# Performance work log

Hardware: AMD Instinct MI355X
Metric: run time of the kernel (lower is better)

Reference implementation:

```python
import jax, jax.numpy as jnp
import numpy as np

NEG = -9e15

def setup_inputs() -> dict:
    key = jax.random.key(0)
    k1, k2, k3, k4 = jax.random.split(key, 4)
    N, F_IN, F_OUT = 8192, 256, 256
    h = jax.random.normal(k1, (N, F_IN), dtype=jnp.float32)
    adj = jax.random.randint(k2, (N, N), 0, 2, dtype=jnp.int32)
    W = jax.random.normal(k3, (F_IN, F_OUT), dtype=jnp.float32) * (1.0 / np.sqrt(F_IN))
    a = jax.random.normal(k4, (2 * F_OUT,), dtype=jnp.float32) * (1.0 / np.sqrt(2 * F_OUT))
    return {"h": h, "adj": adj, "W": W, "a": a}

def reference(h, adj, W, a):
    # Wh: [N, F_out]
    Wh = h @ W
    F_OUT = Wh.shape[1]
    a1, a2 = a[:F_OUT], a[F_OUT:]
    # cat-based score decomposes: e_ij = leaky_relu(a1.Wh_i + a2.Wh_j)
    s1 = Wh @ a1  # [N]
    s2 = Wh @ a2  # [N]
    e = jax.nn.leaky_relu(s1[:, None] + s2[None, :], negative_slope=0.2)  # [N, N]
    e = jnp.where(adj > 0, e, NEG)
    attention = jax.nn.softmax(e, axis=-1)
    # dropout is identity in eval mode
    return attention @ Wh
```

## Files before the change

kernel.cpp:

```cpp
#include <hip/hip_runtime.h>

typedef short s8v  __attribute__((ext_vector_type(8)));
typedef float f4v  __attribute__((ext_vector_type(4)));
typedef int   v4i  __attribute__((ext_vector_type(4)));
typedef float v4f  __attribute__((ext_vector_type(4)));
typedef int   v2i  __attribute__((ext_vector_type(2)));

#define NNODES 8192
#define FDIM   256
#define NJC    4
#define JLEN   2048
#define TROWS  32
#define KSTEP  32
#define NSTEP  64

__device__ __forceinline__ float bf2f(unsigned short u) {
    unsigned int x = ((unsigned int)u) << 16;
    return __builtin_bit_cast(float, x);
}
__device__ __forceinline__ unsigned short f2bf(float f) {
    unsigned int x = __builtin_bit_cast(unsigned int, f);
    x += 0x7fffu + ((x >> 16) & 1u);
    return (unsigned short)(x >> 16);
}
__device__ __forceinline__ int cvt_pk(float lo, float hi) {
    int r;
    asm("v_cvt_pk_bf16_f32 %0, %1, %2" : "=v"(r) : "v"(lo), "v"(hi));
    return r;
}

__device__ __forceinline__ void barrier_lds_only() {
    asm volatile("s_waitcnt lgkmcnt(0)" ::: "memory");
    __builtin_amdgcn_s_barrier();
    asm volatile("" ::: "memory");
}

__global__ __launch_bounds__(256) void prep_kernel(const float* __restrict__ W,
                                                   const float* __restrict__ a,
                                                   unsigned short* __restrict__ WT,
                                                   float* __restrict__ v1,
                                                   float* __restrict__ v2) {
    if (blockIdx.x < 256) {
        int idx = blockIdx.x * 256 + threadIdx.x;
        int r = idx >> 8, c = idx & 255;
        WT[c * 256 + r] = f2bf(W[r * 256 + c]);
    } else {
        __shared__ float r1[256], r2[256];
        int b = blockIdx.x - 256, n = threadIdx.x;
        float w = W[(size_t)b * FDIM + n];
        r1[n] = w * a[n];
        r2[n] = w * a[FDIM + n];
        __syncthreads();
        for (int off = 128; off > 0; off >>= 1) {
            if (n < off) { r1[n] += r1[n + off]; r2[n] += r2[n + off]; }
            __syncthreads();
        }
        if (n == 0) { v1[b] = r1[0]; v2[b] = r2[0]; }
    }
}

__global__ __launch_bounds__(128) void wh_kernel(
    const float* __restrict__ h, const unsigned short* __restrict__ WT,
    const float* __restrict__ v1, const float* __restrict__ v2,
    unsigned short* __restrict__ PB,
    float* __restrict__ s1, float* __restrict__ s2)
{
    __shared__ float v1_lds[FDIM], v2_lds[FDIM];
    int tid = threadIdx.x;
    v1_lds[tid] = v1[tid];       v1_lds[tid + 128] = v1[tid + 128];
    v2_lds[tid] = v2[tid];       v2_lds[tid + 128] = v2[tid + 128];
    __syncthreads();

    int w = tid >> 6, lane = tid & 63, q = lane >> 4, l15 = lane & 15;
    int i_base = blockIdx.x * 32 + w * 16;

    f4v acc[16] = {};
    float s1p = 0.f, s2p = 0.f;

    for (int k0 = 0; k0 < 256; k0 += 32) {
        const float* hp = h + (size_t)(i_base + l15) * FDIM + k0 + q * 8;
        f4v h0 = *(const f4v*)hp;
        f4v h1 = *(const f4v*)(hp + 4);
        union { v4i u; s8v s; } af;
        af.u[0] = cvt_pk(h0[0], h0[1]);
        af.u[1] = cvt_pk(h0[2], h0[3]);
        af.u[2] = cvt_pk(h1[0], h1[1]);
        af.u[3] = cvt_pk(h1[2], h1[3]);
#pragma unroll
        for (int j = 0; j < 4; ++j) {
            s1p += h0[j] * v1_lds[k0 + q * 8 + j] + h1[j] * v1_lds[k0 + q * 8 + 4 + j];
            s2p += h0[j] * v2_lds[k0 + q * 8 + j] + h1[j] * v2_lds[k0 + q * 8 + 4 + j];
        }
#pragma unroll
        for (int t = 0; t < 16; ++t) {
            s8v bf = *(const s8v*)(WT + (size_t)(t * 16 + l15) * FDIM + k0 + q * 8);
            acc[t] = __builtin_amdgcn_mfma_f32_16x16x32_bf16(af.s, bf, acc[t], 0, 0, 0);
        }
    }

    s1p += __shfl_xor(s1p, 16, 64);
    s1p += __shfl_xor(s1p, 32, 64);
    s2p += __shfl_xor(s2p, 16, 64);
    s2p += __shfl_xor(s2p, 32, 64);
    if (lane < 16) {
        s1[i_base + lane] = s1p;
        s2[i_base + lane] = s2p;
    }

#pragma unroll
    for (int t = 0; t < 16; ++t) {
        int i0 = i_base + q * 4;
        size_t a16 = (size_t)((i0 >> 5) * 16 + t) * 512
                   + l15 * 32 + ((i0 >> 3) & 3) * 8 + (i0 & 7);
        v2i pk;
        pk[0] = cvt_pk(acc[t][0], acc[t][1]);
        pk[1] = cvt_pk(acc[t][2], acc[t][3]);
        *(v2i*)(PB + a16) = pk;
    }
}

__global__ __launch_bounds__(256, 4) void attn_partial(
    const int* __restrict__ adj, const unsigned short* __restrict__ PB,
    const float* __restrict__ s1, const float* __restrict__ s2,
    float* __restrict__ Npart, float* __restrict__ dpart)
{
    __shared__ float s2_lds[JLEN];
    __shared__ unsigned short P_lds[2][TROWS * KSTEP];
    __shared__ float dsum_lds[TROWS][8];

    int tid = threadIdx.x;
    int jc = blockIdx.x & 3, rt = blockIdx.x >> 2;
    int j0 = jc * JLEN;

    for (int i = tid; i < JLEN / 4; i += 256)
        ((v4f*)s2_lds)[i] = ((const v4f*)(s2 + j0))[i];

    int m = tid >> 3, idx = tid & 7;
    int row_g = rt * TROWS + m;
    float s1v = s1[row_g];
    const int* arow = adj + (size_t)row_g * NNODES + j0 + idx * 4;
    int q_w = idx >> 1, half = idx & 1;
    int woff = (((q_w * 32 + m) * 8 + half * 4)) ^ (q_w * 16);

    int g = tid >> 6, lane = tid & 63, q = lane >> 4, l15 = lane & 15;
    const unsigned short* pbb = PB + (size_t)(jc * 64) * 16 * 512 + l15 * 32 + q * 8;

    f4v acc[2][4] = {};
    float dsum = 0.0f;

    __syncthreads();

    v4i p0 = __builtin_nontemporal_load((const v4i*)(arow));
    v4i a1 = __builtin_nontemporal_load((const v4i*)(arow + 1 * KSTEP));
    v4i a2 = __builtin_nontemporal_load((const v4i*)(arow + 2 * KSTEP));
    v4i a3 = __builtin_nontemporal_load((const v4i*)(arow + 3 * KSTEP));
    {
        v4f sv = *(const v4f*)&s2_lds[idx * 4];
        float pa[4];
#pragma unroll
        for (int j = 0; j < 4; ++j) {
            float x = s1v + sv[j];
            float p = (p0[j] > 0) ? __expf(fmaxf(x, 0.2f * x)) : 0.0f;
            pa[j] = p; dsum += p;
        }
        v2i pv;
        pv[0] = cvt_pk(pa[0], pa[1]);
        pv[1] = cvt_pk(pa[2], pa[3]);
        *(v2i*)&P_lds[0][woff] = pv;
    }
    barrier_lds_only();

    for (int s = 0; s < NSTEP; ++s) {
        int kn = (s < NSTEP - 4) ? (s + 4) * KSTEP : 0;
        v4i nx = __builtin_nontemporal_load((const v4i*)(arow + kn));

        s8v bf[4];
#pragma unroll
        for (int t = 0; t < 4; ++t)
            bf[t] = *(const s8v*)(pbb + (size_t)(s * 16 + g * 4 + t) * 512);

        if (s < NSTEP - 1) {
            v4f sv = *(const v4f*)&s2_lds[(s + 1) * KSTEP + idx * 4];
            float pa[4];
#pragma unroll
            for (int j = 0; j < 4; ++j) {
                float x = s1v + sv[j];
                float p = (a1[j] > 0) ? __expf(fmaxf(x, 0.2f * x)) : 0.0f;
                pa[j] = p; dsum += p;
            }
            v2i pv;
            pv[0] = cvt_pk(pa[0], pa[1]);
            pv[1] = cvt_pk(pa[2], pa[3]);
            *(v2i*)&P_lds[(s + 1) & 1][woff] = pv;
        }

        const unsigned short* pbuf = P_lds[s & 1];
#pragma unroll
        for (int rh = 0; rh < 2; ++rh) {
            s8v af = *(const s8v*)&pbuf[((q * 32 + rh * 16 + l15) * 8) ^ (q * 16)];
#pragma unroll
            for (int t = 0; t < 4; ++t)
                acc[rh][t] = __builtin_amdgcn_mfma_f32_16x16x32_bf16(af, bf[t], acc[rh][t], 0, 0, 0);
        }

        barrier_lds_only();
        a1 = a2; a2 = a3; a3 = nx;
    }

    dsum_lds[m][idx] = dsum;
    __syncthreads();
    if (tid < TROWS) {
        float d = 0.f;
#pragma unroll
        for (int k = 0; k < 8; ++k) d += dsum_lds[tid][k];
        dpart[jc * NNODES + rt * TROWS + tid] = d;
    }

#pragma unroll
    for (int rh = 0; rh < 2; ++rh)
#pragma unroll
        for (int r = 0; r < 4; ++r) {
            int row = rh * 16 + q * 4 + r;
            float* base = Npart + ((size_t)(jc * NNODES) + rt * TROWS + row) * FDIM;
#pragma unroll
            for (int t = 0; t < 4; ++t)
                __builtin_nontemporal_store(acc[rh][t][r], base + g * 64 + t * 16 + l15);
        }
}

__global__ __launch_bounds__(256) void reduce_kernel(
    const float* __restrict__ Npart, const float* __restrict__ dpart,
    float* __restrict__ out)
{
    int i = blockIdx.x, n = threadIdx.x;
    float d = 0.f, acc = 0.f;
#pragma unroll
    for (int jc = 0; jc < NJC; ++jc) {
        d += dpart[jc * NNODES + i];
        acc += Npart[((size_t)(jc * NNODES) + i) * FDIM + n];
    }
    out[(size_t)i * FDIM + n] = acc / fmaxf(d, 1e-30f);
}

extern "C" void kernel_launch(void* const* d_in, const int* in_sizes, int n_in,
                              void* d_out, int out_size, void* d_ws, size_t ws_size,
                              hipStream_t stream) {
    const float* h   = (const float*)d_in[0];
    const int*   adj = (const int*)d_in[1];
    const float* W   = (const float*)d_in[2];
    const float* a   = (const float*)d_in[3];
    float* out = (float*)d_out;

    char* ws = (char*)d_ws;
    unsigned short* PB = (unsigned short*)ws;
    float* s1 = (float*)(ws + (4u << 20));
    float* s2 = (float*)(ws + (4u << 20) + (32u << 10));
    unsigned short* WT = (unsigned short*)(ws + (4u << 20) + (64u << 10));
    float* v1 = (float*)(ws + (4u << 20) + (192u << 10));
    float* v2 = (float*)(ws + (4u << 20) + (193u << 10));
    float* dpart = (float*)(ws + (5u << 20));
    float* Npart = (float*)(ws + (8u << 20));

    hipLaunchKernelGGL(prep_kernel, dim3(512), dim3(256), 0, stream, W, a, WT, v1, v2);
    hipLaunchKernelGGL(wh_kernel, dim3(256), dim3(128), 0, stream, h, WT, v1, v2, PB, s1, s2);
    hipLaunchKernelGGL(attn_partial, dim3(256 * NJC), dim3(256), 0, stream,
                       adj, PB, s1, s2, Npart, dpart);
    hipLaunchKernelGGL(reduce_kernel, dim3(NNODES), dim3(256), 0, stream, Npart, dpart, out);
}
```

Before: 461.2 us.

## Double attention row tile to 64 and fuse split-K reduction via atomic ticket

Each attention block now handles 64 rows with 512 threads, so every B fragment loaded from PB is reused across four row halves instead of two. Each wave now covers 32 output columns instead of 64. The adjacency prefetch depth drops from four steps to three. The separate reduce kernel is removed: the last of the four column-chunk blocks for a row tile, found with an atomic ticket counter, sums the partials, normalizes, and writes the output. This saves a launch and a pass over the partial buffer, but serializes the final reduction in a few blocks and adds fences.

```diff
diff --git a/kernel.cpp b/kernel.cpp
--- a/kernel.cpp
+++ b/kernel.cpp
@@ -10,14 +10,10 @@
 #define FDIM   256
 #define NJC    4
 #define JLEN   2048
-#define TROWS  32
+#define TROWS  64
 #define KSTEP  32
 #define NSTEP  64
 
-__device__ __forceinline__ float bf2f(unsigned short u) {
-    unsigned int x = ((unsigned int)u) << 16;
-    return __builtin_bit_cast(float, x);
-}
 __device__ __forceinline__ unsigned short f2bf(float f) {
     unsigned int x = __builtin_bit_cast(unsigned int, f);
     x += 0x7fffu + ((x >> 16) & 1u);
@@ -39,8 +35,10 @@
                                                    const float* __restrict__ a,
                                                    unsigned short* __restrict__ WT,
                                                    float* __restrict__ v1,
-                                                   float* __restrict__ v2) {
+                                                   float* __restrict__ v2,
+                                                   int* __restrict__ ticket) {
     if (blockIdx.x < 256) {
+        if (blockIdx.x == 0 && threadIdx.x < 128) ticket[threadIdx.x] = 0;
         int idx = blockIdx.x * 256 + threadIdx.x;
         int r = idx >> 8, c = idx & 255;
         WT[c * 256 + r] = f2bf(W[r * 256 + c]);
@@ -119,33 +117,34 @@
     }
 }
 
-__global__ __launch_bounds__(256, 4) void attn_partial(
+__global__ __launch_bounds__(512, 4) void attn_partial(
     const int* __restrict__ adj, const unsigned short* __restrict__ PB,
     const float* __restrict__ s1, const float* __restrict__ s2,
-    float* __restrict__ Npart, float* __restrict__ dpart)
+    float* __restrict__ Npart, float* __restrict__ dpart,
+    int* __restrict__ ticket, float* __restrict__ out)
 {
     __shared__ float s2_lds[JLEN];
     __shared__ unsigned short P_lds[2][TROWS * KSTEP];
     __shared__ float dsum_lds[TROWS][8];
+    __shared__ int amLast;
 
     int tid = threadIdx.x;
     int jc = blockIdx.x & 3, rt = blockIdx.x >> 2;
     int j0 = jc * JLEN;
 
-    for (int i = tid; i < JLEN / 4; i += 256)
-        ((v4f*)s2_lds)[i] = ((const v4f*)(s2 + j0))[i];
+    ((v4f*)s2_lds)[tid] = ((const v4f*)(s2 + j0))[tid];
 
     int m = tid >> 3, idx = tid & 7;
     int row_g = rt * TROWS + m;
     float s1v = s1[row_g];
     const int* arow = adj + (size_t)row_g * NNODES + j0 + idx * 4;
-    int q_w = idx >> 1, half = idx & 1;
-    int woff = (((q_w * 32 + m) * 8 + half * 4)) ^ (q_w * 16);
+    int qw = idx >> 1, half = idx & 1;
+    int woff = ((qw * 64 + m) * 8 + half * 4) ^ (qw * 16);
 
     int g = tid >> 6, lane = tid & 63, q = lane >> 4, l15 = lane & 15;
     const unsigned short* pbb = PB + (size_t)(jc * 64) * 16 * 512 + l15 * 32 + q * 8;
 
-    f4v acc[2][4] = {};
+    f4v acc[4][2] = {};
     float dsum = 0.0f;
 
     __syncthreads();
@@ -153,7 +152,6 @@
     v4i p0 = __builtin_nontemporal_load((const v4i*)(arow));
     v4i a1 = __builtin_nontemporal_load((const v4i*)(arow + 1 * KSTEP));
     v4i a2 = __builtin_nontemporal_load((const v4i*)(arow + 2 * KSTEP));
-    v4i a3 = __builtin_nontemporal_load((const v4i*)(arow + 3 * KSTEP));
     {
         v4f sv = *(const v4f*)&s2_lds[idx * 4];
         float pa[4];
@@ -171,13 +169,11 @@
     barrier_lds_only();
 
     for (int s = 0; s < NSTEP; ++s) {
-        int kn = (s < NSTEP - 4) ? (s + 4) * KSTEP : 0;
+        int kn = (s < NSTEP - 3) ? (s + 3) * KSTEP : 0;
         v4i nx = __builtin_nontemporal_load((const v4i*)(arow + kn));
 
-        s8v bf[4];
-#pragma unroll
-        for (int t = 0; t < 4; ++t)
-            bf[t] = *(const s8v*)(pbb + (size_t)(s * 16 + g * 4 + t) * 512);
+        s8v bf0 = *(const s8v*)(pbb + (size_t)(s * 16 + g * 2) * 512);
+        s8v bf1 = *(const s8v*)(pbb + (size_t)(s * 16 + g * 2 + 1) * 512);
 
         if (s < NSTEP - 1) {
             v4f sv = *(const v4f*)&s2_lds[(s + 1) * KSTEP + idx * 4];
@@ -196,15 +192,14 @@
 
         const unsigned short* pbuf = P_lds[s & 1];
 #pragma unroll
-        for (int rh = 0; rh < 2; ++rh) {
-            s8v af = *(const s8v*)&pbuf[((q * 32 + rh * 16 + l15) * 8) ^ (q * 16)];
-#pragma unroll
-            for (int t = 0; t < 4; ++t)
-                acc[rh][t] = __builtin_amdgcn_mfma_f32_16x16x32_bf16(af, bf[t], acc[rh][t], 0, 0, 0);
+        for (int rh = 0; rh < 4; ++rh) {
+            s8v af = *(const s8v*)&pbuf[((q * 64 + rh * 16 + l15) * 8) ^ (q * 16)];
+            acc[rh][0] = __builtin_amdgcn_mfma_f32_16x16x32_bf16(af, bf0, acc[rh][0], 0, 0, 0);
+            acc[rh][1] = __builtin_amdgcn_mfma_f32_16x16x32_bf16(af, bf1, acc[rh][1], 0, 0, 0);
         }
 
         barrier_lds_only();
-        a1 = a2; a2 = a3; a3 = nx;
+        a1 = a2; a2 = nx;
     }
 
     dsum_lds[m][idx] = dsum;
@@ -217,29 +212,39 @@
     }
 
 #pragma unroll
-    for (int rh = 0; rh < 2; ++rh)
+    for (int rh = 0; rh < 4; ++rh)
 #pragma unroll
         for (int r = 0; r < 4; ++r) {
             int row = rh * 16 + q * 4 + r;
             float* base = Npart + ((size_t)(jc * NNODES) + rt * TROWS + row) * FDIM;
-#pragma unroll
-            for (int t = 0; t < 4; ++t)
-                __builtin_nontemporal_store(acc[rh][t][r], base + g * 64 + t * 16 + l15);
-        }
-}
-
-__global__ __launch_bounds__(256) void reduce_kernel(
-    const float* __restrict__ Npart, const float* __restrict__ dpart,
-    float* __restrict__ out)
-{
-    int i = blockIdx.x, n = threadIdx.x;
-    float d = 0.f, acc = 0.f;
-#pragma unroll
-    for (int jc = 0; jc < NJC; ++jc) {
-        d += dpart[jc * NNODES + i];
-        acc += Npart[((size_t)(jc * NNODES) + i) * FDIM + n];
-    }
-    out[(size_t)i * FDIM + n] = acc / fmaxf(d, 1e-30f);
+            base[g * 32 + l15]      = acc[rh][0][r];
+            base[g * 32 + 16 + l15] = acc[rh][1][r];
+        }
+
+    __threadfence();
+    __syncthreads();
+    if (tid == 0) amLast = (atomicAdd(&ticket[rt], 1) == NJC - 1);
+    __syncthreads();
+    if (amLast) {
+        __threadfence();
+        if (tid < TROWS) {
+            float dd = 0.f;
+#pragma unroll
+            for (int jcc = 0; jcc < NJC; ++jcc)
+                dd += dpart[jcc * NNODES + rt * TROWS + tid];
+            dsum_lds[tid][0] = dd;
+        }
+        __syncthreads();
+        for (int e = tid; e < TROWS * FDIM; e += 512) {
+            int row = e >> 8, col = e & 255;
+            float sacc = 0.f;
+#pragma unroll
+            for (int jcc = 0; jcc < NJC; ++jcc)
+                sacc += Npart[((size_t)(jcc * NNODES) + rt * TROWS + row) * FDIM + col];
+            out[((size_t)(rt * TROWS + row)) * FDIM + col] =
+                sacc / fmaxf(dsum_lds[row][0], 1e-30f);
+        }
+    }
 }
 
 extern "C" void kernel_launch(void* const* d_in, const int* in_sizes, int n_in,
@@ -259,11 +264,11 @@
     float* v1 = (float*)(ws + (4u << 20) + (192u << 10));
     float* v2 = (float*)(ws + (4u << 20) + (193u << 10));
     float* dpart = (float*)(ws + (5u << 20));
+    int* ticket  = (int*)(ws + (5u << 20) + (128u << 10));
     float* Npart = (float*)(ws + (8u << 20));
 
-    hipLaunchKernelGGL(prep_kernel, dim3(512), dim3(256), 0, stream, W, a, WT, v1, v2);
+    hipLaunchKernelGGL(prep_kernel, dim3(512), dim3(256), 0, stream, W, a, WT, v1, v2, ticket);
     hipLaunchKernelGGL(wh_kernel, dim3(256), dim3(128), 0, stream, h, WT, v1, v2, PB, s1, s2);
-    hipLaunchKernelGGL(attn_partial, dim3(256 * NJC), dim3(256), 0, stream,
-                       adj, PB, s1, s2, Npart, dpart);
-    hipLaunchKernelGGL(reduce_kernel, dim3(NNODES), dim3(256), 0, stream, Npart, dpart, out);
-}
+    hipLaunchKernelGGL(attn_partial, dim3(128 * NJC), dim3(512), 0, stream,
+                       adj, PB, s1, s2, Npart, dpart, ticket, out);
+}
```

Measured after the change: 624.0 us. 1.35x slower.

## Compute attention probabilities directly in MFMA registers, dropping the LDS exchange and barriers

Applied to the files above, without the earlier changes.

The attention kernel no longer builds the bf16 probability tile cooperatively in LDS. Each wave now loads adjacency values and computes exp scores straight into the MFMA A-operand register layout. The row tile doubles to 64 rows, launch bounds move to 2 blocks per CU, and the grid is halved. Adjacency and Wh fragments are double-buffered in registers across an unrolled pair of steps. This removes the per-step LDS writes, reads and block barriers, and reuses each PB fragment across four row groups. The cost is that every wave redundantly loads the same adjacency rows and recomputes the same exponentials, with a shallower prefetch and more register pressure.

```diff
diff --git a/kernel.cpp b/kernel.cpp
--- a/kernel.cpp
+++ b/kernel.cpp
@@ -10,14 +10,11 @@
 #define FDIM   256
 #define NJC    4
 #define JLEN   2048
-#define TROWS  32
+#define TROWS  64
 #define KSTEP  32
 #define NSTEP  64
-
-__device__ __forceinline__ float bf2f(unsigned short u) {
-    unsigned int x = ((unsigned int)u) << 16;
-    return __builtin_bit_cast(float, x);
-}
+#define RSTR   ((size_t)16 * NNODES)
+
 __device__ __forceinline__ unsigned short f2bf(float f) {
     unsigned int x = __builtin_bit_cast(unsigned int, f);
     x += 0x7fffu + ((x >> 16) & 1u);
@@ -27,12 +24,6 @@
     int r;
     asm("v_cvt_pk_bf16_f32 %0, %1, %2" : "=v"(r) : "v"(lo), "v"(hi));
     return r;
-}
-
-__device__ __forceinline__ void barrier_lds_only() {
-    asm volatile("s_waitcnt lgkmcnt(0)" ::: "memory");
-    __builtin_amdgcn_s_barrier();
-    asm volatile("" ::: "memory");
 }
 
 __global__ __launch_bounds__(256) void prep_kernel(const float* __restrict__ W,
@@ -119,14 +110,12 @@
     }
 }
 
-__global__ __launch_bounds__(256, 4) void attn_partial(
+__global__ __launch_bounds__(256, 2) void attn_partial(
     const int* __restrict__ adj, const unsigned short* __restrict__ PB,
     const float* __restrict__ s1, const float* __restrict__ s2,
     float* __restrict__ Npart, float* __restrict__ dpart)
 {
     __shared__ float s2_lds[JLEN];
-    __shared__ unsigned short P_lds[2][TROWS * KSTEP];
-    __shared__ float dsum_lds[TROWS][8];
 
     int tid = threadIdx.x;
     int jc = blockIdx.x & 3, rt = blockIdx.x >> 2;
@@ -135,89 +124,85 @@
     for (int i = tid; i < JLEN / 4; i += 256)
         ((v4f*)s2_lds)[i] = ((const v4f*)(s2 + j0))[i];
 
-    int m = tid >> 3, idx = tid & 7;
-    int row_g = rt * TROWS + m;
-    float s1v = s1[row_g];
-    const int* arow = adj + (size_t)row_g * NNODES + j0 + idx * 4;
-    int q_w = idx >> 1, half = idx & 1;
-    int woff = (((q_w * 32 + m) * 8 + half * 4)) ^ (q_w * 16);
-
     int g = tid >> 6, lane = tid & 63, q = lane >> 4, l15 = lane & 15;
-    const unsigned short* pbb = PB + (size_t)(jc * 64) * 16 * 512 + l15 * 32 + q * 8;
-
-    f4v acc[2][4] = {};
-    float dsum = 0.0f;
+
+    float s1r[4];
+#pragma unroll
+    for (int rh = 0; rh < 4; ++rh) s1r[rh] = s1[rt * TROWS + rh * 16 + l15];
+
+    const unsigned short* pbb = PB + (size_t)(jc * NSTEP) * 16 * 512 + l15 * 32 + q * 8;
+    const int* arow = adj + (size_t)(rt * TROWS + l15) * NNODES + j0 + q * 8;
+
+    f4v acc[4][4] = {};
+    float dsum4[4] = {0.f, 0.f, 0.f, 0.f};
 
     __syncthreads();
 
-    v4i p0 = __builtin_nontemporal_load((const v4i*)(arow));
-    v4i a1 = __builtin_nontemporal_load((const v4i*)(arow + 1 * KSTEP));
-    v4i a2 = __builtin_nontemporal_load((const v4i*)(arow + 2 * KSTEP));
-    v4i a3 = __builtin_nontemporal_load((const v4i*)(arow + 3 * KSTEP));
-    {
-        v4f sv = *(const v4f*)&s2_lds[idx * 4];
-        float pa[4];
-#pragma unroll
-        for (int j = 0; j < 4; ++j) {
-            float x = s1v + sv[j];
-            float p = (p0[j] > 0) ? __expf(fmaxf(x, 0.2f * x)) : 0.0f;
-            pa[j] = p; dsum += p;
-        }
-        v2i pv;
-        pv[0] = cvt_pk(pa[0], pa[1]);
-        pv[1] = cvt_pk(pa[2], pa[3]);
-        *(v2i*)&P_lds[0][woff] = pv;
-    }
-    barrier_lds_only();
-
-    for (int s = 0; s < NSTEP; ++s) {
-        int kn = (s < NSTEP - 4) ? (s + 4) * KSTEP : 0;
-        v4i nx = __builtin_nontemporal_load((const v4i*)(arow + kn));
-
-        s8v bf[4];
-#pragma unroll
-        for (int t = 0; t < 4; ++t)
-            bf[t] = *(const s8v*)(pbb + (size_t)(s * 16 + g * 4 + t) * 512);
-
-        if (s < NSTEP - 1) {
-            v4f sv = *(const v4f*)&s2_lds[(s + 1) * KSTEP + idx * 4];
-            float pa[4];
-#pragma unroll
-            for (int j = 0; j < 4; ++j) {
-                float x = s1v + sv[j];
-                float p = (a1[j] > 0) ? __expf(fmaxf(x, 0.2f * x)) : 0.0f;
-                pa[j] = p; dsum += p;
-            }
-            v2i pv;
-            pv[0] = cvt_pk(pa[0], pa[1]);
-            pv[1] = cvt_pk(pa[2], pa[3]);
-            *(v2i*)&P_lds[(s + 1) & 1][woff] = pv;
-        }
-
-        const unsigned short* pbuf = P_lds[s & 1];
-#pragma unroll
-        for (int rh = 0; rh < 2; ++rh) {
-            s8v af = *(const s8v*)&pbuf[((q * 32 + rh * 16 + l15) * 8) ^ (q * 16)];
-#pragma unroll
-            for (int t = 0; t < 4; ++t)
-                acc[rh][t] = __builtin_amdgcn_mfma_f32_16x16x32_bf16(af, bf[t], acc[rh][t], 0, 0, 0);
-        }
-
-        barrier_lds_only();
-        a1 = a2; a2 = a3; a3 = nx;
-    }
-
-    dsum_lds[m][idx] = dsum;
-    __syncthreads();
-    if (tid < TROWS) {
-        float d = 0.f;
-#pragma unroll
-        for (int k = 0; k < 8; ++k) d += dsum_lds[tid][k];
-        dpart[jc * NNODES + rt * TROWS + tid] = d;
-    }
-
-#pragma unroll
-    for (int rh = 0; rh < 2; ++rh)
+    v4i aA[4][2], aB[4][2];
+#pragma unroll
+    for (int rh = 0; rh < 4; ++rh) {
+        const int* pp = arow + rh * RSTR;
+        aA[rh][0] = *(const v4i*)(pp);
+        aA[rh][1] = *(const v4i*)(pp + 4);
+        aB[rh][0] = *(const v4i*)(pp + KSTEP);
+        aB[rh][1] = *(const v4i*)(pp + KSTEP + 4);
+    }
+    s8v bfA[4], bfB[4];
+#pragma unroll
+    for (int t = 0; t < 4; ++t)
+        bfA[t] = *(const s8v*)(pbb + (size_t)(g * 4 + t) * 512);
+
+#define ASTEP(S, AC, BC, BN) do {                                             \
+    int sc = (S);                                                             \
+    v4f svA = *(const v4f*)&s2_lds[sc * KSTEP + q * 8];                       \
+    v4f svB = *(const v4f*)&s2_lds[sc * KSTEP + q * 8 + 4];                   \
+    int sb = (sc + 1 < NSTEP) ? sc + 1 : 0;                                   \
+    _Pragma("unroll")                                                         \
+    for (int t = 0; t < 4; ++t)                                               \
+        BN[t] = *(const s8v*)(pbb + (size_t)(sb * 16 + g * 4 + t) * 512);     \
+    int sn = (sc + 2 < NSTEP) ? sc + 2 : 0;                                   \
+    _Pragma("unroll")                                                         \
+    for (int rh = 0; rh < 4; ++rh) {                                          \
+        float pa[8];                                                          \
+        _Pragma("unroll")                                                     \
+        for (int j = 0; j < 4; ++j) {                                         \
+            float x = s1r[rh] + svA[j];                                       \
+            pa[j] = (AC[rh][0][j] > 0) ? __expf(fmaxf(x, 0.2f * x)) : 0.0f;   \
+            float x2 = s1r[rh] + svB[j];                                      \
+            pa[4 + j] = (AC[rh][1][j] > 0) ? __expf(fmaxf(x2, 0.2f * x2)) : 0.0f; \
+            dsum4[rh] += pa[j] + pa[4 + j];                                   \
+        }                                                                     \
+        union { v4i u; s8v s; } af;                                           \
+        af.u[0] = cvt_pk(pa[0], pa[1]);  af.u[1] = cvt_pk(pa[2], pa[3]);      \
+        af.u[2] = cvt_pk(pa[4], pa[5]);  af.u[3] = cvt_pk(pa[6], pa[7]);      \
+        _Pragma("unroll")                                                     \
+        for (int t = 0; t < 4; ++t)                                           \
+            acc[rh][t] = __builtin_amdgcn_mfma_f32_16x16x32_bf16(af.s, BC[t], acc[rh][t], 0, 0, 0); \
+        const int* pp = arow + rh * RSTR + (size_t)sn * KSTEP;                \
+        AC[rh][0] = *(const v4i*)(pp);                                        \
+        AC[rh][1] = *(const v4i*)(pp + 4);                                    \
+    }                                                                         \
+} while (0)
+
+    for (int s = 0; s < NSTEP; s += 2) {
+        ASTEP(s,     aA, bfA, bfB);
+        ASTEP(s + 1, aB, bfB, bfA);
+    }
+#undef ASTEP
+
+#pragma unroll
+    for (int rh = 0; rh < 4; ++rh) {
+        dsum4[rh] += __shfl_xor(dsum4[rh], 16, 64);
+        dsum4[rh] += __shfl_xor(dsum4[rh], 32, 64);
+    }
+    if (g == 0 && lane < 16) {
+#pragma unroll
+        for (int rh = 0; rh < 4; ++rh)
+            dpart[jc * NNODES + rt * TROWS + rh * 16 + lane] = dsum4[rh];
+    }
+
+#pragma unroll
+    for (int rh = 0; rh < 4; ++rh)
 #pragma unroll
         for (int r = 0; r < 4; ++r) {
             int row = rh * 16 + q * 4 + r;
@@ -263,7 +248,7 @@
 
     hipLaunchKernelGGL(prep_kernel, dim3(512), dim3(256), 0, stream, W, a, WT, v1, v2);
     hipLaunchKernelGGL(wh_kernel, dim3(256), dim3(128), 0, stream, h, WT, v1, v2, PB, s1, s2);
-    hipLaunchKernelGGL(attn_partial, dim3(256 * NJC), dim3(256), 0, stream,
+    hipLaunchKernelGGL(attn_partial, dim3(128 * NJC), dim3(256), 0, stream,
                        adj, PB, s1, s2, Npart, dpart);
     hipLaunchKernelGGL(reduce_kernel, dim3(NNODES), dim3(256), 0, stream, Npart, dpart, out);
 }
```

After: 489.5 us. +6.1%, slower.
